# Optimization experiments

Hardware: AMD Instinct MI355X
Metric: run time of the kernel (lower is better)

The kernel has to match this reference:

```python
import jax, jax.numpy as jnp
import numpy as np

N_NODES = 100000
K = 10
VOCAB = 100000
FEAT_DIM = 128


def setup_inputs() -> dict:
    key = jax.random.key(0)
    k1, k2 = jax.random.split(key)
    weight = jax.random.normal(k1, (VOCAB, FEAT_DIM), dtype=jnp.float32)
    neighbor_idx = jax.random.randint(k2, (N_NODES, K), 0, VOCAB, dtype=jnp.int64)
    return {"weight": weight, "neighbor_idx": neighbor_idx}


def reference(weight, neighbor_idx):
    # Mean aggregator: gather neighbor embeddings and average per node.
    # Equivalent to the original's (mask / num_neigh).mm(gathered_features)
    # with a fixed fan-out K per node.
    gathered = weight[neighbor_idx]          # [N, K, D]
    return jnp.mean(gathered, axis=1)        # [N, D]
```

## Files before the change

kernel.cpp:

```cpp
#include <hip/hip_runtime.h>


#define AGG_K 10
#define AGG_D 128

__global__ __launch_bounds__(256) void Aggregator_26439818674919_kernel(
    const float* __restrict__ weight,
    const int* __restrict__ nidx,
    float* __restrict__ out,
    int n_nodes) {
  const int tid  = blockIdx.x * 256 + threadIdx.x;
  const int node = tid >> 5;
  const int lane = tid & 31;
  if (node >= n_nodes) return;

  const int ibase = node * AGG_K;
  float4 acc = make_float4(0.f, 0.f, 0.f, 0.f);
#pragma unroll
  for (int k = 0; k < AGG_K; ++k) {
    const int idx = nidx[ibase + k];
    const float4 v = *reinterpret_cast<const float4*>(
        &weight[(size_t)idx * AGG_D + lane * 4]);
    acc.x += v.x; acc.y += v.y; acc.z += v.z; acc.w += v.w;
  }
  const float s = 1.0f / AGG_K;
  acc.x *= s; acc.y *= s; acc.z *= s; acc.w *= s;
  *reinterpret_cast<float4*>(&out[(size_t)node * AGG_D + lane * 4]) = acc;
}

extern "C" void kernel_launch(void* const* d_in, const int* in_sizes, int n_in,
                              void* d_out, int out_size, void* d_ws, size_t ws_size,
                              hipStream_t stream) {
  const float* weight = (const float*)d_in[0];
  const int*   nidx   = (const int*)d_in[1];
  float*       out    = (float*)d_out;

  const int n_nodes = in_sizes[1] / AGG_K;
  const int total_threads = n_nodes * 32;
  const int blocks = (total_threads + 255) / 256;

  Aggregator_26439818674919_kernel<<<blocks, 256, 0, stream>>>(
      weight, nidx, out, n_nodes);
}
```

Measured before the change: 154.3 us.

## Make gather kernel persistent with index prefetch and inline-asm loads

Result: no change. 157.2 us (+1.9%).

```diff
diff --git a/kernel.cpp b/kernel.cpp
--- a/kernel.cpp
+++ b/kernel.cpp
@@ -4,28 +4,69 @@
 #define AGG_K 10
 #define AGG_D 128
 
+typedef float f32x4 __attribute__((ext_vector_type(4)));
+typedef int   i32x2 __attribute__((ext_vector_type(2)));
+
 __global__ __launch_bounds__(256) void Aggregator_26439818674919_kernel(
     const float* __restrict__ weight,
     const int* __restrict__ nidx,
     float* __restrict__ out,
-    int n_nodes) {
+    int n_nodes, int nslots) {
   const int tid  = blockIdx.x * 256 + threadIdx.x;
-  const int node = tid >> 5;
+  int cur = tid >> 5;
   const int lane = tid & 31;
-  if (node >= n_nodes) return;
+  if (cur >= n_nodes) return;
 
-  const int ibase = node * AGG_K;
-  float4 acc = make_float4(0.f, 0.f, 0.f, 0.f);
-#pragma unroll
-  for (int k = 0; k < AGG_K; ++k) {
-    const int idx = nidx[ibase + k];
-    const float4 v = *reinterpret_cast<const float4*>(
-        &weight[(size_t)idx * AGG_D + lane * 4]);
-    acc.x += v.x; acc.y += v.y; acc.z += v.z; acc.w += v.w;
+  const unsigned lane_off = (unsigned)(lane * 4);
+  i32x2 I0, I1, I2, I3, I4;
+  f32x4 v0, v1, v2, v3, v4, v5, v6, v7, v8, v9;
+
+#define AGG_IDX_LD(node_)                                                    \
+  {                                                                          \
+    const int* ip_ = nidx + (size_t)(node_) * AGG_K;                         \
+    asm volatile("global_load_dwordx2 %0, %1, off" : "=v"(I0) : "v"(ip_));   \
+    asm volatile("global_load_dwordx2 %0, %1, off" : "=v"(I1) : "v"(ip_+2)); \
+    asm volatile("global_load_dwordx2 %0, %1, off" : "=v"(I2) : "v"(ip_+4)); \
+    asm volatile("global_load_dwordx2 %0, %1, off" : "=v"(I3) : "v"(ip_+6)); \
+    asm volatile("global_load_dwordx2 %0, %1, off" : "=v"(I4) : "v"(ip_+8)); \
   }
-  const float s = 1.0f / AGG_K;
-  acc.x *= s; acc.y *= s; acc.z *= s; acc.w *= s;
-  *reinterpret_cast<float4*>(&out[(size_t)node * AGG_D + lane * 4]) = acc;
+
+#define AGG_GATHER(ii, dst)                                                  \
+  {                                                                          \
+    const float* p_ = weight + ((unsigned)(ii) * AGG_D + lane_off);          \
+    asm volatile("global_load_dwordx4 %0, %1, off" : "=v"(dst) : "v"(p_));   \
+  }
+#define AGG_GATHER_ALL()                                                     \
+  AGG_GATHER(I0[0], v0) AGG_GATHER(I0[1], v1) AGG_GATHER(I1[0], v2)          \
+  AGG_GATHER(I1[1], v3) AGG_GATHER(I2[0], v4) AGG_GATHER(I2[1], v5)          \
+  AGG_GATHER(I3[0], v6) AGG_GATHER(I3[1], v7) AGG_GATHER(I4[0], v8)          \
+  AGG_GATHER(I4[1], v9)
+
+  AGG_IDX_LD(cur);
+  asm volatile("s_waitcnt vmcnt(0)" ::: "memory");
+  __builtin_amdgcn_sched_barrier(0);
+  AGG_GATHER_ALL();
+
+  for (;;) {
+    const int nxt = cur + nslots;
+    AGG_IDX_LD(nxt < n_nodes ? nxt : cur);
+    asm volatile("s_waitcnt vmcnt(5)" ::: "memory");
+    __builtin_amdgcn_sched_barrier(0);
+
+    f32x4 acc = ((v0 + v1) + (v2 + v3)) +
+                (((v4 + v5) + (v6 + v7)) + (v8 + v9));
+    acc *= (1.0f / AGG_K);
+    float* op_ = out + (size_t)cur * AGG_D + lane_off;
+    asm volatile("global_store_dwordx4 %0, %1, off nt"
+                 :: "v"(op_), "v"(acc) : "memory");
+
+    if (nxt >= n_nodes) break;
+
+    asm volatile("s_waitcnt vmcnt(1)" ::: "memory");
+    __builtin_amdgcn_sched_barrier(0);
+    cur = nxt;
+    AGG_GATHER_ALL();
+  }
 }
 
 extern "C" void kernel_launch(void* const* d_in, const int* in_sizes, int n_in,
@@ -36,9 +77,9 @@
   float*       out    = (float*)d_out;
 
   const int n_nodes = in_sizes[1] / AGG_K;
-  const int total_threads = n_nodes * 32;
-  const int blocks = (total_threads + 255) / 256;
+  const int blocks  = 2048;
+  const int nslots  = blocks * 256 / 32;
 
   Aggregator_26439818674919_kernel<<<blocks, 256, 0, stream>>>(
-      weight, nidx, out, n_nodes);
+      weight, nidx, out, n_nodes, nslots);
 }
```
